# Kernel optimization log

Measured on AMD Instinct MI355X. Metric: run time of the kernel, lower is better.

The kernel has to match this reference:

```python
import jax, jax.numpy as jnp
import numpy as np

B, N, K, V = 16, 256, 2048, 768

def setup_inputs() -> dict:
    key = jax.random.key(0)
    k1, k2 = jax.random.split(key)
    inputs = jax.random.normal(k1, (B, N, V), dtype=jnp.float32)
    prototypes = jax.random.normal(k2, (K, V), dtype=jnp.float32)
    return {"inputs": inputs, "prototypes": prototypes}

def reference(inputs, prototypes):
    # distances[b,n,k] = sum_v (inputs[b,n,v] - prototypes[k,v])**2
    x_sq = jnp.sum(inputs * inputs, axis=-1, keepdims=True)          # [B,N,1]
    p_sq = jnp.sum(prototypes * prototypes, axis=-1)                  # [K]
    xp = jnp.einsum("bnv,kv->bnk", inputs, prototypes)               # [B,N,K]
    distances = x_sq + p_sq[None, None, :] - 2.0 * xp
    return (distances, prototypes)
```

## Files before the change

### kernel.cpp

```cpp
#include <hip/hip_runtime.h>
#include <hip/hip_bf16.h>
#include <stdint.h>

#define Bdim 16
#define Ndim 256
#define Kdim 2048
#define Vdim 768
#define Mdim 4096

#define BM 256
#define BN 128
#define BK 64
#define NT (Vdim / BK)
#define ASZ (BM * BK)
#define BSZ (BN * BK)

typedef __attribute__((ext_vector_type(8))) short short8;
typedef __attribute__((ext_vector_type(4))) float f32x4;

struct alignas(8) bf16x4 { __hip_bfloat16 x, y, z, w; };

#define CFENCE asm volatile("" ::: "memory")

__device__ __forceinline__ void gld_lds16(const void* g, void* l) {
    __builtin_amdgcn_global_load_lds((const __attribute__((address_space(1))) void*)g,
                                     (__attribute__((address_space(3))) void*)l, 16, 0, 0);
}

__global__ __launch_bounds__(256) void rowconv_all(const float* __restrict__ x,
                                                   const float* __restrict__ p,
                                                   __hip_bfloat16* __restrict__ Ab,
                                                   __hip_bfloat16* __restrict__ Pb,
                                                   float* __restrict__ xsq,
                                                   float* __restrict__ psq,
                                                   float* __restrict__ proto_out) {
    const int row = blockIdx.x * 4 + (threadIdx.x >> 6);
    const int lane = threadIdx.x & 63;

    const float* src;
    __hip_bfloat16* dstb;
    float* sq;
    float* cpy = nullptr;
    if (row < Mdim) {
        src = x + (size_t)row * Vdim;
        dstb = Ab + (size_t)row * Vdim;
        sq = xsq + row;
    } else {
        const int r = row - Mdim;
        src = p + (size_t)r * Vdim;
        dstb = Pb + (size_t)r * Vdim;
        sq = psq + r;
        cpy = proto_out + (size_t)r * Vdim;
    }

    float s = 0.f;
#pragma unroll
    for (int j = 0; j < Vdim / 256; ++j) {
        float4 v = *reinterpret_cast<const float4*>(src + j * 256 + lane * 4);
        s += v.x * v.x + v.y * v.y + v.z * v.z + v.w * v.w;
        bf16x4 b;
        b.x = __float2bfloat16(v.x); b.y = __float2bfloat16(v.y);
        b.z = __float2bfloat16(v.z); b.w = __float2bfloat16(v.w);
        *reinterpret_cast<bf16x4*>(dstb + j * 256 + lane * 4) = b;
        if (cpy) *reinterpret_cast<float4*>(cpy + j * 256 + lane * 4) = v;
    }
#pragma unroll
    for (int off = 32; off > 0; off >>= 1) s += __shfl_down(s, off);
    if (lane == 0) *sq = s;
}

__global__ __launch_bounds__(512) void gemm_dist(const __hip_bfloat16* __restrict__ Ab,
                                                 const __hip_bfloat16* __restrict__ Pb,
                                                 const float* __restrict__ xsq,
                                                 const float* __restrict__ psq,
                                                 float* __restrict__ out) {
    __shared__ __hip_bfloat16 As[3][ASZ];
    __shared__ __hip_bfloat16 Bs[3][BSZ];

    const int t = threadIdx.x;
    const int lane = t & 63;
    const int wave = t >> 6;
    const int wr = wave >> 1;
    const int wc = wave & 1;
    const int fr = lane & 15;
    const int g  = lane >> 4;

    const int wg = (blockIdx.x & 7) * 32 + (blockIdx.x >> 3);
    const int bm = wg >> 4;
    const int bn = wg & 15;
    const int m0 = bm * BM, n0 = bn * BN;

    const int srow = t >> 3;
    const int scol = ((t & 7) ^ (srow & 7)) * 8;
    const __hip_bfloat16* Ag = Ab + (size_t)(m0 + srow) * Vdim + scol;
    const __hip_bfloat16* Bg = Pb + (size_t)(n0 + srow) * Vdim + scol;
    const int ldsw = (t >> 6) * 512;

    int offA[4][2], offB[4][2];
#pragma unroll
    for (int i = 0; i < 4; ++i)
#pragma unroll
        for (int s = 0; s < 2; ++s) {
            const int slot = (((s * 4 + g) ^ (fr & 7)) * 16);
            offA[i][s] = (wr * 64 + i * 16 + fr) * 128 + slot;
            offB[i][s] = (wc * 64 + i * 16 + fr) * 128 + slot;
        }

    f32x4 acc[4][4] = {};

    auto stgA = [&](int buf, int kt, int q) {
        gld_lds16(Ag + (size_t)q * 64 * Vdim + kt * BK, (void*)(&As[buf][q * 4096 + ldsw]));
    };
    auto stgB = [&](int buf, int kt, int q) {
        gld_lds16(Bg + (size_t)q * 64 * Vdim + kt * BK, (void*)(&Bs[buf][q * 4096 + ldsw]));
    };

#pragma unroll
    for (int p = 0; p < 3; ++p) {
        stgA(p, p, 0); stgA(p, p, 1); stgA(p, p, 2); stgA(p, p, 3);
        stgB(p, p, 0); stgB(p, p, 1);
    }
    asm volatile("s_waitcnt vmcnt(12)" ::: "memory");
    __builtin_amdgcn_s_barrier();
    CFENCE;

    int cb = 0, cs = 2;
    for (int kt = 0; kt < NT; ++kt) {
        const char* Ap = (const char*)&As[cb][0];
        const char* Bp = (const char*)&Bs[cb][0];
        const bool doStage = (kt >= 1 && kt <= NT - 3);

        short8 bq[4][2], a0[2][2];
#pragma unroll
        for (int j = 0; j < 4; ++j)
#pragma unroll
            for (int s = 0; s < 2; ++s)
                bq[j][s] = *reinterpret_cast<const short8*>(Bp + offB[j][s]);
#pragma unroll
        for (int i = 0; i < 2; ++i)
#pragma unroll
            for (int s = 0; s < 2; ++s)
                a0[i][s] = *reinterpret_cast<const short8*>(Ap + offA[i][s]);
        if (doStage) { stgA(cs, kt + 2, 0); stgA(cs, kt + 2, 1); stgA(cs, kt + 2, 2); }
        CFENCE;
        __builtin_amdgcn_s_barrier();
        CFENCE;
        __builtin_amdgcn_s_setprio(1);
#pragma unroll
        for (int s = 0; s < 2; ++s)
#pragma unroll
            for (int i = 0; i < 2; ++i)
#pragma unroll
                for (int j = 0; j < 4; ++j)
                    acc[i][j] = __builtin_amdgcn_mfma_f32_16x16x32_bf16(a0[i][s], bq[j][s], acc[i][j], 0, 0, 0);
        __builtin_amdgcn_s_setprio(0);
        CFENCE;
        __builtin_amdgcn_s_barrier();
        CFENCE;

        short8 a1[2][2];
#pragma unroll
        for (int i = 0; i < 2; ++i)
#pragma unroll
            for (int s = 0; s < 2; ++s)
                a1[i][s] = *reinterpret_cast<const short8*>(Ap + offA[i + 2][s]);
        if (doStage) { stgA(cs, kt + 2, 3); stgB(cs, kt + 2, 0); stgB(cs, kt + 2, 1); }
        CFENCE;
        __builtin_amdgcn_s_barrier();
        CFENCE;
        __builtin_amdgcn_s_setprio(1);
#pragma unroll
        for (int s = 0; s < 2; ++s)
#pragma unroll
            for (int i = 0; i < 2; ++i)
#pragma unroll
                for (int j = 0; j < 4; ++j)
                    acc[i + 2][j] = __builtin_amdgcn_mfma_f32_16x16x32_bf16(a1[i][s], bq[j][s], acc[i + 2][j], 0, 0, 0);
        __builtin_amdgcn_s_setprio(0);
        CFENCE;
        if (kt <= NT - 3)      asm volatile("s_waitcnt vmcnt(6)" ::: "memory");
        else if (kt == NT - 2) asm volatile("s_waitcnt vmcnt(0)" ::: "memory");
        __builtin_amdgcn_s_barrier();
        CFENCE;

        cb = (cb == 2) ? 0 : cb + 1;
        cs = (cs == 2) ? 0 : cs + 1;
    }

    const int fq = g;
    float ps[4];
#pragma unroll
    for (int j = 0; j < 4; ++j) ps[j] = psq[n0 + wc * 64 + j * 16 + fr];
#pragma unroll
    for (int i = 0; i < 4; ++i) {
#pragma unroll
        for (int r = 0; r < 4; ++r) {
            const int m = m0 + wr * 64 + i * 16 + fq * 4 + r;
            const float xs = xsq[m];
            float* orow = out + (size_t)m * Kdim + n0 + wc * 64;
#pragma unroll
            for (int j = 0; j < 4; ++j)
                orow[j * 16 + fr] = xs + ps[j] - 2.0f * acc[i][j][r];
        }
    }
}

extern "C" void kernel_launch(void* const* d_in, const int* in_sizes, int n_in,
                              void* d_out, int out_size, void* d_ws, size_t ws_size,
                              hipStream_t stream) {
    const float* x = (const float*)d_in[0];
    const float* p = (const float*)d_in[1];
    float* out = (float*)d_out;

    char* ws = (char*)d_ws;
    __hip_bfloat16* Ab = (__hip_bfloat16*)ws;
    __hip_bfloat16* Pb = (__hip_bfloat16*)(ws + 6291456);
    float* xsq = (float*)(ws + 6291456 + 3145728);
    float* psq = (float*)(ws + 6291456 + 3145728 + 16384);

    rowconv_all<<<(Mdim + Kdim) / 4, 256, 0, stream>>>(x, p, Ab, Pb, xsq, psq,
                                                       out + (size_t)Mdim * Kdim);
    gemm_dist<<<(Mdim / BM) * (Kdim / BN), 512, 0, stream>>>(Ab, Pb, xsq, psq, out);
}
```

Baseline: 33.11 us.

## Quantize inputs and prototypes to int8 with per-row scales and use i8 MFMA

```diff
diff --git a/kernel.cpp b/kernel.cpp
--- a/kernel.cpp
+++ b/kernel.cpp
@@ -2,23 +2,17 @@
 #include <hip/hip_bf16.h>
 #include <stdint.h>
 
-#define Bdim 16
-#define Ndim 256
 #define Kdim 2048
 #define Vdim 768
 #define Mdim 4096
 
 #define BM 256
 #define BN 128
-#define BK 64
+#define BK 128
 #define NT (Vdim / BK)
-#define ASZ (BM * BK)
-#define BSZ (BN * BK)
-
-typedef __attribute__((ext_vector_type(8))) short short8;
-typedef __attribute__((ext_vector_type(4))) float f32x4;
-
-struct alignas(8) bf16x4 { __hip_bfloat16 x, y, z, w; };
+
+typedef __attribute__((ext_vector_type(4))) int  i32x4;
+typedef __attribute__((ext_vector_type(16))) int i32x16;
 
 #define CFENCE asm volatile("" ::: "memory")
 
@@ -27,98 +21,112 @@
                                      (__attribute__((address_space(3))) void*)l, 16, 0, 0);
 }
 
-__global__ __launch_bounds__(256) void rowconv_all(const float* __restrict__ x,
-                                                   const float* __restrict__ p,
-                                                   __hip_bfloat16* __restrict__ Ab,
-                                                   __hip_bfloat16* __restrict__ Pb,
-                                                   float* __restrict__ xsq,
-                                                   float* __restrict__ psq,
-                                                   float* __restrict__ proto_out) {
+__global__ __launch_bounds__(256) void rowquant(const float* __restrict__ x,
+                                                const float* __restrict__ p,
+                                                int8_t* __restrict__ Aq,
+                                                int8_t* __restrict__ Pq,
+                                                float* __restrict__ xsq,
+                                                float* __restrict__ psq,
+                                                float* __restrict__ sxa,
+                                                float* __restrict__ spa,
+                                                float* __restrict__ proto_out) {
     const int row = blockIdx.x * 4 + (threadIdx.x >> 6);
     const int lane = threadIdx.x & 63;
 
     const float* src;
-    __hip_bfloat16* dstb;
-    float* sq;
-    float* cpy = nullptr;
+    int8_t* dq;
+    float *sq, *sc, *cpy = nullptr;
     if (row < Mdim) {
-        src = x + (size_t)row * Vdim;
-        dstb = Ab + (size_t)row * Vdim;
-        sq = xsq + row;
+        src = x + (size_t)row * Vdim; dq = Aq + (size_t)row * Vdim;
+        sq = xsq + row; sc = sxa + row;
     } else {
         const int r = row - Mdim;
-        src = p + (size_t)r * Vdim;
-        dstb = Pb + (size_t)r * Vdim;
-        sq = psq + r;
-        cpy = proto_out + (size_t)r * Vdim;
-    }
-
-    float s = 0.f;
-#pragma unroll
-    for (int j = 0; j < Vdim / 256; ++j) {
-        float4 v = *reinterpret_cast<const float4*>(src + j * 256 + lane * 4);
-        s += v.x * v.x + v.y * v.y + v.z * v.z + v.w * v.w;
-        bf16x4 b;
-        b.x = __float2bfloat16(v.x); b.y = __float2bfloat16(v.y);
-        b.z = __float2bfloat16(v.z); b.w = __float2bfloat16(v.w);
-        *reinterpret_cast<bf16x4*>(dstb + j * 256 + lane * 4) = b;
-        if (cpy) *reinterpret_cast<float4*>(cpy + j * 256 + lane * 4) = v;
-    }
-#pragma unroll
-    for (int off = 32; off > 0; off >>= 1) s += __shfl_down(s, off);
-    if (lane == 0) *sq = s;
-}
-
-__global__ __launch_bounds__(512) void gemm_dist(const __hip_bfloat16* __restrict__ Ab,
-                                                 const __hip_bfloat16* __restrict__ Pb,
-                                                 const float* __restrict__ xsq,
-                                                 const float* __restrict__ psq,
-                                                 float* __restrict__ out) {
-    __shared__ __hip_bfloat16 As[3][ASZ];
-    __shared__ __hip_bfloat16 Bs[3][BSZ];
+        src = p + (size_t)r * Vdim; dq = Pq + (size_t)r * Vdim;
+        sq = psq + r; sc = spa + r; cpy = proto_out + (size_t)r * Vdim;
+    }
+
+    float4 v[3];
+    float s = 0.f, mx = 0.f;
+#pragma unroll
+    for (int j = 0; j < 3; ++j) {
+        v[j] = *reinterpret_cast<const float4*>(src + j * 256 + lane * 4);
+        s += v[j].x * v[j].x + v[j].y * v[j].y + v[j].z * v[j].z + v[j].w * v[j].w;
+        mx = fmaxf(mx, fmaxf(fmaxf(fabsf(v[j].x), fabsf(v[j].y)),
+                             fmaxf(fabsf(v[j].z), fabsf(v[j].w))));
+        if (cpy) *reinterpret_cast<float4*>(cpy + j * 256 + lane * 4) = v[j];
+    }
+#pragma unroll
+    for (int off = 32; off > 0; off >>= 1) {
+        s += __shfl_xor(s, off);
+        mx = fmaxf(mx, __shfl_xor(mx, off));
+    }
+    mx = fmaxf(mx, 1e-20f);
+    const float inv = 127.0f / mx;
+#pragma unroll
+    for (int j = 0; j < 3; ++j) {
+        int q0 = min(127, max(-127, __float2int_rn(v[j].x * inv)));
+        int q1 = min(127, max(-127, __float2int_rn(v[j].y * inv)));
+        int q2 = min(127, max(-127, __float2int_rn(v[j].z * inv)));
+        int q3 = min(127, max(-127, __float2int_rn(v[j].w * inv)));
+        int packed = (q0 & 0xff) | ((q1 & 0xff) << 8) | ((q2 & 0xff) << 16) | (q3 << 24);
+        *reinterpret_cast<int*>(dq + j * 256 + lane * 4) = packed;
+    }
+    if (lane == 0) { *sq = s; *sc = mx * (1.0f / 127.0f); }
+}
+
+__global__ __launch_bounds__(512) void gemm_dist_i8(const int8_t* __restrict__ Aq,
+                                                    const int8_t* __restrict__ Pq,
+                                                    const float* __restrict__ xsq,
+                                                    const float* __restrict__ psq,
+                                                    const float* __restrict__ sxa,
+                                                    const float* __restrict__ spa,
+                                                    float* __restrict__ out) {
+    __shared__ int8_t As[3][BM * BK];
+    __shared__ int8_t Bs[3][BN * BK];
 
     const int t = threadIdx.x;
     const int lane = t & 63;
     const int wave = t >> 6;
     const int wr = wave >> 1;
     const int wc = wave & 1;
-    const int fr = lane & 15;
-    const int g  = lane >> 4;
+    const int ln31 = lane & 31;
+    const int lh = lane >> 5;
 
     const int wg = (blockIdx.x & 7) * 32 + (blockIdx.x >> 3);
-    const int bm = wg >> 4;
-    const int bn = wg & 15;
+    const int bm = wg >> 4, bn = wg & 15;
     const int m0 = bm * BM, n0 = bn * BN;
 
     const int srow = t >> 3;
-    const int scol = ((t & 7) ^ (srow & 7)) * 8;
-    const __hip_bfloat16* Ag = Ab + (size_t)(m0 + srow) * Vdim + scol;
-    const __hip_bfloat16* Bg = Pb + (size_t)(n0 + srow) * Vdim + scol;
-    const int ldsw = (t >> 6) * 512;
-
-    int offA[4][2], offB[4][2];
-#pragma unroll
-    for (int i = 0; i < 4; ++i)
-#pragma unroll
-        for (int s = 0; s < 2; ++s) {
-            const int slot = (((s * 4 + g) ^ (fr & 7)) * 16);
-            offA[i][s] = (wr * 64 + i * 16 + fr) * 128 + slot;
-            offB[i][s] = (wc * 64 + i * 16 + fr) * 128 + slot;
+    const int scol = ((t & 7) ^ (srow & 7)) * 16;
+    const int8_t* Ag = Aq + (size_t)(m0 + srow) * Vdim + scol;
+    const int8_t* Bg = Pq + (size_t)(n0 + srow) * Vdim + scol;
+    const int ldsw = wave * 1024;
+
+    int offA[2][4], offB[2][4];
+#pragma unroll
+    for (int mt = 0; mt < 2; ++mt)
+#pragma unroll
+        for (int ks = 0; ks < 4; ++ks) {
+            const int k16 = ks * 2 + lh;
+            const int rA = wr * 64 + mt * 32 + ln31;
+            const int rB = wc * 64 + mt * 32 + ln31;
+            offA[mt][ks] = rA * BK + ((k16 ^ (rA & 7)) * 16);
+            offB[mt][ks] = rB * BK + ((k16 ^ (rB & 7)) * 16);
         }
 
-    f32x4 acc[4][4] = {};
+    i32x16 acc[2][2] = {};
 
     auto stgA = [&](int buf, int kt, int q) {
-        gld_lds16(Ag + (size_t)q * 64 * Vdim + kt * BK, (void*)(&As[buf][q * 4096 + ldsw]));
+        gld_lds16(Ag + (size_t)q * 64 * Vdim + kt * BK, (void*)(&As[buf][q * 8192 + ldsw]));
     };
     auto stgB = [&](int buf, int kt, int q) {
-        gld_lds16(Bg + (size_t)q * 64 * Vdim + kt * BK, (void*)(&Bs[buf][q * 4096 + ldsw]));
+        gld_lds16(Bg + (size_t)q * 64 * Vdim + kt * BK, (void*)(&Bs[buf][q * 8192 + ldsw]));
     };
 
 #pragma unroll
-    for (int p = 0; p < 3; ++p) {
-        stgA(p, p, 0); stgA(p, p, 1); stgA(p, p, 2); stgA(p, p, 3);
-        stgB(p, p, 0); stgB(p, p, 1);
+    for (int pb = 0; pb < 3; ++pb) {
+        stgA(pb, pb, 0); stgA(pb, pb, 1); stgA(pb, pb, 2); stgA(pb, pb, 3);
+        stgB(pb, pb, 0); stgB(pb, pb, 1);
     }
     asm volatile("s_waitcnt vmcnt(12)" ::: "memory");
     __builtin_amdgcn_s_barrier();
@@ -126,56 +134,48 @@
 
     int cb = 0, cs = 2;
     for (int kt = 0; kt < NT; ++kt) {
-        const char* Ap = (const char*)&As[cb][0];
-        const char* Bp = (const char*)&Bs[cb][0];
+        const int8_t* Ap = &As[cb][0];
+        const int8_t* Bp = &Bs[cb][0];
         const bool doStage = (kt >= 1 && kt <= NT - 3);
 
-        short8 bq[4][2], a0[2][2];
-#pragma unroll
-        for (int j = 0; j < 4; ++j)
-#pragma unroll
-            for (int s = 0; s < 2; ++s)
-                bq[j][s] = *reinterpret_cast<const short8*>(Bp + offB[j][s]);
-#pragma unroll
-        for (int i = 0; i < 2; ++i)
-#pragma unroll
-            for (int s = 0; s < 2; ++s)
-                a0[i][s] = *reinterpret_cast<const short8*>(Ap + offA[i][s]);
+        i32x4 bq[2][4], a0[4];
+#pragma unroll
+        for (int nt = 0; nt < 2; ++nt)
+#pragma unroll
+            for (int ks = 0; ks < 4; ++ks)
+                bq[nt][ks] = *reinterpret_cast<const i32x4*>(Bp + offB[nt][ks]);
+#pragma unroll
+        for (int ks = 0; ks < 4; ++ks)
+            a0[ks] = *reinterpret_cast<const i32x4*>(Ap + offA[0][ks]);
         if (doStage) { stgA(cs, kt + 2, 0); stgA(cs, kt + 2, 1); stgA(cs, kt + 2, 2); }
         CFENCE;
         __builtin_amdgcn_s_barrier();
         CFENCE;
         __builtin_amdgcn_s_setprio(1);
 #pragma unroll
-        for (int s = 0; s < 2; ++s)
-#pragma unroll
-            for (int i = 0; i < 2; ++i)
-#pragma unroll
-                for (int j = 0; j < 4; ++j)
-                    acc[i][j] = __builtin_amdgcn_mfma_f32_16x16x32_bf16(a0[i][s], bq[j][s], acc[i][j], 0, 0, 0);
+        for (int ks = 0; ks < 4; ++ks)
+#pragma unroll
+            for (int nt = 0; nt < 2; ++nt)
+                acc[0][nt] = __builtin_amdgcn_mfma_i32_32x32x32_i8(a0[ks], bq[nt][ks], acc[0][nt], 0, 0, 0);
         __builtin_amdgcn_s_setprio(0);
         CFENCE;
         __builtin_amdgcn_s_barrier();
         CFENCE;
 
-        short8 a1[2][2];
-#pragma unroll
-        for (int i = 0; i < 2; ++i)
-#pragma unroll
-            for (int s = 0; s < 2; ++s)
-                a1[i][s] = *reinterpret_cast<const short8*>(Ap + offA[i + 2][s]);
+        i32x4 a1[4];
+#pragma unroll
+        for (int ks = 0; ks < 4; ++ks)
+            a1[ks] = *reinterpret_cast<const i32x4*>(Ap + offA[1][ks]);
         if (doStage) { stgA(cs, kt + 2, 3); stgB(cs, kt + 2, 0); stgB(cs, kt + 2, 1); }
         CFENCE;
         __builtin_amdgcn_s_barrier();
         CFENCE;
         __builtin_amdgcn_s_setprio(1);
 #pragma unroll
-        for (int s = 0; s < 2; ++s)
-#pragma unroll
-            for (int i = 0; i < 2; ++i)
-#pragma unroll
-                for (int j = 0; j < 4; ++j)
-                    acc[i + 2][j] = __builtin_amdgcn_mfma_f32_16x16x32_bf16(a1[i][s], bq[j][s], acc[i + 2][j], 0, 0, 0);
+        for (int ks = 0; ks < 4; ++ks)
+#pragma unroll
+            for (int nt = 0; nt < 2; ++nt)
+                acc[1][nt] = __builtin_amdgcn_mfma_i32_32x32x32_i8(a1[ks], bq[nt][ks], acc[1][nt], 0, 0, 0);
         __builtin_amdgcn_s_setprio(0);
         CFENCE;
         if (kt <= NT - 3)      asm volatile("s_waitcnt vmcnt(6)" ::: "memory");
@@ -187,22 +187,26 @@
         cs = (cs == 2) ? 0 : cs + 1;
     }
 
-    const int fq = g;
-    float ps[4];
-#pragma unroll
-    for (int j = 0; j < 4; ++j) ps[j] = psq[n0 + wc * 64 + j * 16 + fr];
-#pragma unroll
-    for (int i = 0; i < 4; ++i) {
-#pragma unroll
-        for (int r = 0; r < 4; ++r) {
-            const int m = m0 + wr * 64 + i * 16 + fq * 4 + r;
-            const float xs = xsq[m];
-            float* orow = out + (size_t)m * Kdim + n0 + wc * 64;
-#pragma unroll
-            for (int j = 0; j < 4; ++j)
-                orow[j * 16 + fr] = xs + ps[j] - 2.0f * acc[i][j][r];
+    float ps_[2], sp_[2];
+    int col_[2];
+#pragma unroll
+    for (int nt = 0; nt < 2; ++nt) {
+        col_[nt] = n0 + wc * 64 + nt * 32 + ln31;
+        ps_[nt] = psq[col_[nt]];
+        sp_[nt] = spa[col_[nt]];
+    }
+#pragma unroll
+    for (int mt = 0; mt < 2; ++mt)
+#pragma unroll
+        for (int reg = 0; reg < 16; ++reg) {
+            const int row = m0 + wr * 64 + mt * 32 + (reg & 3) + 8 * (reg >> 2) + 4 * lh;
+            const float xs = xsq[row];
+            const float m2sx = -2.0f * sxa[row];
+#pragma unroll
+            for (int nt = 0; nt < 2; ++nt)
+                out[(size_t)row * Kdim + col_[nt]] =
+                    xs + ps_[nt] + m2sx * sp_[nt] * (float)acc[mt][nt][reg];
         }
-    }
 }
 
 extern "C" void kernel_launch(void* const* d_in, const int* in_sizes, int n_in,
@@ -213,12 +217,14 @@
     float* out = (float*)d_out;
 
     char* ws = (char*)d_ws;
-    __hip_bfloat16* Ab = (__hip_bfloat16*)ws;
-    __hip_bfloat16* Pb = (__hip_bfloat16*)(ws + 6291456);
-    float* xsq = (float*)(ws + 6291456 + 3145728);
-    float* psq = (float*)(ws + 6291456 + 3145728 + 16384);
-
-    rowconv_all<<<(Mdim + Kdim) / 4, 256, 0, stream>>>(x, p, Ab, Pb, xsq, psq,
-                                                       out + (size_t)Mdim * Kdim);
-    gemm_dist<<<(Mdim / BM) * (Kdim / BN), 512, 0, stream>>>(Ab, Pb, xsq, psq, out);
-}
+    int8_t* Aq = (int8_t*)ws;
+    int8_t* Pq = (int8_t*)(ws + 3145728);
+    float* xsq = (float*)(ws + 4718592);
+    float* psq = (float*)(ws + 4734976);
+    float* sxa = (float*)(ws + 4743168);
+    float* spa = (float*)(ws + 4759552);
+
+    rowquant<<<(Mdim + Kdim) / 4, 256, 0, stream>>>(x, p, Aq, Pq, xsq, psq, sxa, spa,
+                                                    out + (size_t)Mdim * Kdim);
+    gemm_dist_i8<<<(Mdim / BM) * (Kdim / BN), 512, 0, stream>>>(Aq, Pq, xsq, psq, sxa, spa, out);
+}
```

Result: faster. 27.86 us (-15.9%).
